# Kernel optimization log

Hardware: AMD Instinct MI355X
Metric: run time of the kernel (lower is better)

## Reference

```python
import jax, jax.numpy as jnp
import numpy as np

B, T, C, H = 2, 2048, 1024, 16
HD = C // H  # head_dim = 64

def _rope(x, cos, sin):
    # x: [B,H,T,HD]; cos/sin: [T,HD//2]
    x2 = x.reshape(*x.shape[:-1], HD // 2, 2)
    x0, x1 = x2[..., 0], x2[..., 1]
    # complex multiply (x0 + i x1) * (cos + i sin)
    o0 = x0 * cos - x1 * sin
    o1 = x0 * sin + x1 * cos
    return jnp.stack([o0, o1], axis=-1).reshape(x.shape)

def setup_inputs() -> dict:
    key = jax.random.key(0)
    k1, k2, k3 = jax.random.split(key, 3)
    x = jax.random.normal(k1, (B, T, C), dtype=jnp.float32)
    w_qkv = jax.random.normal(k2, (C, 3 * C), dtype=jnp.float32) * (1.0 / np.sqrt(C))
    w_proj = jax.random.normal(k3, (C, C), dtype=jnp.float32) * (1.0 / np.sqrt(C))
    # standard RoPE frequencies: theta_j = 10000^(-2j/HD), angles t*theta_j
    inv_freq = 1.0 / (10000.0 ** (np.arange(0, HD, 2, dtype=np.float32) / HD))  # [HD//2]
    ang = np.arange(T, dtype=np.float32)[:, None] * inv_freq[None, :]           # [T,HD//2]
    return {"x": x, "w_qkv": w_qkv, "w_proj": w_proj,
            "freqs_cos": jnp.asarray(np.cos(ang)), "freqs_sin": jnp.asarray(np.sin(ang))}

def reference(x, w_qkv, w_proj, freqs_cos, freqs_sin):
    qkv = x @ w_qkv                                   # [B,T,3C]
    q, k, v = jnp.split(qkv, 3, axis=-1)
    def heads(t):
        return t.reshape(B, T, H, HD).transpose(0, 2, 1, 3)  # [B,H,T,HD]
    q, k, v = heads(q), heads(k), heads(v)
    q = _rope(q, freqs_cos, freqs_sin)
    k = _rope(k, freqs_cos, freqs_sin)
    scores = jnp.einsum('bhqd,bhkd->bhqk', q, k) * (1.0 / np.sqrt(HD))
    causal = jnp.tril(jnp.ones((T, T), dtype=bool))
    scores = jnp.where(causal, scores, jnp.finfo(scores.dtype).min)
    attn = jax.nn.softmax(scores, axis=-1)
    y = jnp.einsum('bhqk,bhkd->bhqd', attn, v)        # [B,H,T,HD]
    y = y.transpose(0, 2, 1, 3).reshape(B, T, C)
    return y @ w_proj
```

## Files before the change

kernel.cpp:

```cpp
#include <hip/hip_runtime.h>

typedef float  floatx4 __attribute__((ext_vector_type(4)));
typedef _Float16 half8 __attribute__((ext_vector_type(8)));
typedef _Float16 half4v __attribute__((ext_vector_type(4)));
typedef _Float16 half2v __attribute__((ext_vector_type(2)));

__device__ __forceinline__ void gld16(const void* g, void* l) {
    __builtin_amdgcn_global_load_lds(
        (const __attribute__((address_space(1))) void*)g,
        (__attribute__((address_space(3))) void*)l, 16, 0, 0);
}

__global__ __launch_bounds__(256) void conv_x_kernel(const float* __restrict__ x,
                                                     _Float16* __restrict__ xh) {
    int i = blockIdx.x * 256 + threadIdx.x;
    float4 v = ((const float4*)x)[i];
    half4v o = { (_Float16)v.x, (_Float16)v.y, (_Float16)v.z, (_Float16)v.w };
    ((half4v*)xh)[i] = o;
}

__global__ __launch_bounds__(256) void transpose_f32f16(const float* __restrict__ W,
                                                        _Float16* __restrict__ WT,
                                                        int K, int N) {
    __shared__ _Float16 t[64][72];
    int n0 = blockIdx.x * 64, k0 = blockIdx.y * 64;
    int c = threadIdx.x & 63, r4 = threadIdx.x >> 6;
    for (int rr = 0; rr < 64; rr += 4) {
        int k = k0 + rr + r4;
        t[rr + r4][c] = (_Float16)W[(size_t)k * N + n0 + c];
    }
    __syncthreads();
    for (int rr = 0; rr < 64; rr += 4) {
        int n = n0 + rr + r4;
        WT[(size_t)n * K + k0 + c] = t[c][rr + r4];
    }
}

__global__ __launch_bounds__(256) void gemm_tn(const _Float16* __restrict__ A,
                                               const _Float16* __restrict__ BT,
                                               _Float16* __restrict__ Cf16,
                                               float* __restrict__ Cf32,
                                               int M, int N, int K) {
    __shared__ __align__(16) _Float16 sAB[2 * 128 * 32];
    _Float16* sA = sAB;
    _Float16* sB = sAB + 128 * 32;

    const int tid  = threadIdx.x;
    const int wave = tid >> 6, lane = tid & 63;
    const int lrow = lane & 15, quad = lane >> 4;
    const int bm = blockIdx.x * 128, bn = blockIdx.y * 128;
    const int waveM = (wave >> 1) * 64, waveN = (wave & 1) * 64;

    floatx4 acc[4][4] = {};

    const int r0 = tid >> 2,          k80 = (tid & 3) * 8;
    const int r1 = (tid + 256) >> 2,  k81 = ((tid + 256) & 3) * 8;
    _Float16* lA0 = sA + (wave * 64) * 8;
    _Float16* lA1 = sA + (wave * 64 + 256) * 8;
    _Float16* lB0 = sB + (wave * 64) * 8;
    _Float16* lB1 = sB + (wave * 64 + 256) * 8;
    const _Float16* A0 = A + (size_t)(bm + r0) * K + k80;
    const _Float16* A1 = A + (size_t)(bm + r1) * K + k81;
    const _Float16* B0 = BT + (size_t)(bn + r0) * K + k80;
    const _Float16* B1 = BT + (size_t)(bn + r1) * K + k81;

    for (int k0 = 0; k0 < K; k0 += 32) {
        gld16(A0 + k0, lA0);
        gld16(A1 + k0, lA1);
        gld16(B0 + k0, lB0);
        gld16(B1 + k0, lB1);
        __syncthreads();

        half8 aF[4], bF[4];
#pragma unroll
        for (int mt = 0; mt < 4; ++mt)
            aF[mt] = *(const half8*)&sA[(waveM + mt * 16 + lrow) * 32 + quad * 8];
#pragma unroll
        for (int nt = 0; nt < 4; ++nt)
            bF[nt] = *(const half8*)&sB[(waveN + nt * 16 + lrow) * 32 + quad * 8];
#pragma unroll
        for (int mt = 0; mt < 4; ++mt)
#pragma unroll
            for (int nt = 0; nt < 4; ++nt)
                acc[mt][nt] = __builtin_amdgcn_mfma_f32_16x16x32_f16(
                    aF[mt], bF[nt], acc[mt][nt], 0, 0, 0);
        __syncthreads();
    }

    if (Cf16) {
        const int PS = 132;
#pragma unroll
        for (int pass = 0; pass < 4; ++pass) {
            if ((wave >> 1) == (pass >> 1)) {
#pragma unroll
                for (int mt2 = 0; mt2 < 2; ++mt2) {
                    int mt = (pass & 1) * 2 + mt2;
#pragma unroll
                    for (int nt = 0; nt < 4; ++nt)
#pragma unroll
                        for (int r = 0; r < 4; ++r)
                            sAB[(mt2 * 16 + quad * 4 + r) * PS + waveN + nt * 16 + lrow] =
                                (_Float16)acc[mt][nt][r];
                }
            }
            __syncthreads();
            {
                int row = tid >> 3, c0 = (tid & 7) * 16;
                const uint4* src = (const uint4*)&sAB[row * PS + c0];
                uint4 d0 = src[0], d1 = src[1];
                uint4* dst = (uint4*)&Cf16[(size_t)(bm + pass * 32 + row) * N + bn + c0];
                dst[0] = d0; dst[1] = d1;
            }
            __syncthreads();
        }
    } else {
#pragma unroll
        for (int mt = 0; mt < 4; ++mt)
#pragma unroll
            for (int nt = 0; nt < 4; ++nt)
#pragma unroll
                for (int r = 0; r < 4; ++r) {
                    int row = bm + waveM + mt * 16 + quad * 4 + r;
                    int col = bn + waveN + nt * 16 + lrow;
                    Cf32[(size_t)row * N + col] = acc[mt][nt][r];
                }
    }
}

__global__ __launch_bounds__(256) void rope_vt(const _Float16* __restrict__ qkv,
                                               const float* __restrict__ fc,
                                               const float* __restrict__ fs,
                                               _Float16* __restrict__ qh,
                                               _Float16* __restrict__ kh,
                                               _Float16* __restrict__ vt) {
    __shared__ _Float16 s[64][72];
    const int bh = blockIdx.y, b = bh >> 4, h = bh & 15;
    const int t0 = blockIdx.x * 64;
    const int tid = threadIdx.x;

    {
        int c4 = (tid & 15) * 4;
        int j0 = c4 >> 1;
        int rr = tid >> 4;
#pragma unroll
        for (int pass = 0; pass < 4; ++pass) {
            int tt = t0 + pass * 16 + rr;
            const _Float16* src = qkv + (size_t)(b * 2048 + tt) * 3072 + h * 64 + c4;
            float c0 = fc[tt * 32 + j0],     s0 = fs[tt * 32 + j0];
            float c1 = fc[tt * 32 + j0 + 1], s1 = fs[tt * 32 + j0 + 1];
            half4v qv = *(const half4v*)(src);
            half4v kv = *(const half4v*)(src + 1024);
            half4v qo, ko;
            {
                float x0 = (float)qv[0], x1 = (float)qv[1];
                qo[0] = (_Float16)(x0 * c0 - x1 * s0); qo[1] = (_Float16)(x0 * s0 + x1 * c0);
                x0 = (float)qv[2]; x1 = (float)qv[3];
                qo[2] = (_Float16)(x0 * c1 - x1 * s1); qo[3] = (_Float16)(x0 * s1 + x1 * c1);
                x0 = (float)kv[0]; x1 = (float)kv[1];
                ko[0] = (_Float16)(x0 * c0 - x1 * s0); ko[1] = (_Float16)(x0 * s0 + x1 * c0);
                x0 = (float)kv[2]; x1 = (float)kv[3];
                ko[2] = (_Float16)(x0 * c1 - x1 * s1); ko[3] = (_Float16)(x0 * s1 + x1 * c1);
            }
            size_t o = ((size_t)bh * 2048 + tt) * 64 + c4;
            *(half4v*)&qh[o] = qo;
            *(half4v*)&kh[o] = ko;
        }
    }
    {
        int c = tid & 63, r4 = tid >> 6;
        const _Float16* srcv = qkv + 2048 + h * 64;
        for (int rr = 0; rr < 64; rr += 4)
            s[rr + r4][c] = srcv[(size_t)(b * 2048 + t0 + rr + r4) * 3072 + c];
        __syncthreads();
        for (int rr = 0; rr < 64; rr += 4)
            vt[((size_t)bh * 64 + rr + r4) * 2048 + t0 + c] = s[c][rr + r4];
    }
}

__global__ __launch_bounds__(256, 6) void attn_sk(const _Float16* __restrict__ Q,
                                                  const _Float16* __restrict__ Kk,
                                                  const _Float16* __restrict__ Vt,
                                                  _Float16* __restrict__ Y,
                                                  _Float16* __restrict__ Opart,
                                                  float* __restrict__ lpart) {
    __shared__ __align__(16) _Float16 sK[64 * 64];
    __shared__ __align__(16) _Float16 sV[64 * 64];
    __shared__ __align__(16) _Float16 sP[64 * 72];

    const int bh = blockIdx.x, b = bh >> 4, h = bh & 15;
    const int u = blockIdx.y;
    int qt, k0, k1, slot = 0; bool direct;
    if (u < 16)              { qt = 16 + u;  k0 = 0;  k1 = 15; direct = false; slot = (qt - 16) * 2; }
    else { int i = (u - 16) >> 1;
        if (((u - 16) & 1) == 0) { qt = 15 - i; k0 = 0;  k1 = qt; direct = true; }
        else                     { qt = 31 - i; k0 = 16; k1 = qt; direct = false; slot = (qt - 16) * 2 + 1; }
    }

    const int tid = threadIdx.x;
    const int wave = tid >> 6, lane = tid & 63;
    const int lq = lane & 15, quad = lane >> 4;

    const _Float16* Kbase = Kk + (size_t)bh * 2048 * 64;
    const _Float16* Vbase = Vt + (size_t)bh * 64 * 2048;

    const _Float16 qscale = (_Float16)(0.125f * 1.44269504f);
    half8 qF[2];
    {
        const _Float16* Qp = Q + ((size_t)bh * 2048 + qt * 64 + wave * 16 + lq) * 64;
#pragma unroll
        for (int ks = 0; ks < 2; ++ks)
            qF[ks] = (*(const half8*)(Qp + ks * 32 + quad * 8)) * qscale;
    }

    floatx4 O[4] = {};
    float lacc = 0.f;

    for (int kt = k0; kt <= k1; ++kt) {
        const _Float16* kb = Kbase + (size_t)kt * 64 * 64;
        const _Float16* vb = Vbase + kt * 64;
#pragma unroll
        for (int hlf = 0; hlf < 2; ++hlf) {
            int s = tid + hlf * 256;
            int row = s >> 3;
            int ccg = (s & 7) ^ (row & 7);
            gld16(kb + row * 64 + ccg * 8, sK + s * 8);
            gld16(vb + (size_t)row * 2048 + ccg * 8, sV + s * 8);
        }
        __syncthreads();

        floatx4 St[4];
#pragma unroll
        for (int kt4 = 0; kt4 < 4; ++kt4) {
            floatx4 s = { -12.f, -12.f, -12.f, -12.f };
#pragma unroll
            for (int ks = 0; ks < 2; ++ks) {
                half8 kf = *(const half8*)&sK[(kt4 * 16 + lq) * 64 +
                                              (((ks * 4 + quad) ^ (lq & 7)) * 8)];
                s = __builtin_amdgcn_mfma_f32_16x16x32_f16(kf, qF[ks], s, 0, 0, 0);
            }
            St[kt4] = s;
        }
        if (kt == qt) {
#pragma unroll
            for (int kt4 = 0; kt4 < 4; ++kt4)
#pragma unroll
                for (int r = 0; r < 4; ++r)
                    if (kt4 * 16 + quad * 4 + r > wave * 16 + lq) St[kt4][r] = -1e30f;
        }
#pragma unroll
        for (int kt4 = 0; kt4 < 4; ++kt4)
#pragma unroll
            for (int r = 0; r < 4; ++r)
                St[kt4][r] = __builtin_amdgcn_exp2f(St[kt4][r]);
        lacc += (St[0][0] + St[0][1] + St[0][2] + St[0][3])
              + (St[1][0] + St[1][1] + St[1][2] + St[1][3])
              + (St[2][0] + St[2][1] + St[2][2] + St[2][3])
              + (St[3][0] + St[3][1] + St[3][2] + St[3][3]);

        _Float16* pw = (_Float16*)&sP[(wave * 16 + lq) * 72];
#pragma unroll
        for (int kt4 = 0; kt4 < 4; ++kt4) {
            half4v pk = { (_Float16)St[kt4][0], (_Float16)St[kt4][1],
                          (_Float16)St[kt4][2], (_Float16)St[kt4][3] };
            *(half4v*)(pw + kt4 * 16 + quad * 4) = pk;
        }
        half8 aP[2];
#pragma unroll
        for (int ks = 0; ks < 2; ++ks)
            aP[ks] = *(const half8*)(pw + ks * 32 + quad * 8);
#pragma unroll
        for (int nt = 0; nt < 4; ++nt)
#pragma unroll
            for (int ks = 0; ks < 2; ++ks) {
                half8 vf = *(const half8*)&sV[(nt * 16 + lq) * 64 +
                                              (((ks * 4 + quad) ^ (lq & 7)) * 8)];
                O[nt] = __builtin_amdgcn_mfma_f32_16x16x32_f16(aP[ks], vf, O[nt], 0, 0, 0);
            }
        __syncthreads();
    }

    float l = lacc;
    l += __shfl_xor(l, 16);
    l += __shfl_xor(l, 32);

    if (direct) {
        float invl = 1.0f / l;
#pragma unroll
        for (int r = 0; r < 4; ++r) {
            float iv = __shfl(invl, (lane & 48) | (quad * 4 + r));
            int q = qt * 64 + wave * 16 + quad * 4 + r;
            size_t rowoff = ((size_t)b * 2048 + q) * 1024 + h * 64;
#pragma unroll
            for (int nt = 0; nt < 4; ++nt)
                Y[rowoff + nt * 16 + lq] = (_Float16)(O[nt][r] * iv);
        }
    } else {
        int gslot = bh * 32 + slot;
        _Float16* op = Opart + (size_t)gslot * 4096;
#pragma unroll
        for (int r = 0; r < 4; ++r) {
            int row = wave * 16 + quad * 4 + r;
#pragma unroll
            for (int nt = 0; nt < 4; ++nt)
                op[row * 64 + nt * 16 + lq] = (_Float16)O[nt][r];
        }
        if (quad == 0)
            lpart[gslot * 64 + wave * 16 + lq] = l;
    }
}

__global__ __launch_bounds__(256) void attn_reduce(const _Float16* __restrict__ Opart,
                                                   const float* __restrict__ lpart,
                                                   _Float16* __restrict__ Y) {
    const int bh = blockIdx.x, b = bh >> 4, h = bh & 15;
    const int qx = blockIdx.y, qt = 16 + qx;
    const int g0 = (bh * 16 + qx) * 2, g1 = g0 + 1;
    const int t = threadIdx.x;
    const int row = t >> 2, cs = (t & 3) * 16;

    const _Float16* p0 = Opart + (size_t)g0 * 4096 + row * 64 + cs;
    const _Float16* p1 = Opart + (size_t)g1 * 4096 + row * 64 + cs;
    float invl = 1.0f / (lpart[g0 * 64 + row] + lpart[g1 * 64 + row]);

    half8 a0 = *(const half8*)p0, a1 = *(const half8*)(p0 + 8);
    half8 b0 = *(const half8*)p1, b1 = *(const half8*)(p1 + 8);
    half8 o0, o1;
#pragma unroll
    for (int i = 0; i < 8; ++i) {
        o0[i] = (_Float16)(((float)a0[i] + (float)b0[i]) * invl);
        o1[i] = (_Float16)(((float)a1[i] + (float)b1[i]) * invl);
    }
    _Float16* y = Y + ((size_t)b * 2048 + qt * 64 + row) * 1024 + h * 64 + cs;
    *(half8*)y = o0;
    *(half8*)(y + 8) = o1;
}

extern "C" void kernel_launch(void* const* d_in, const int* in_sizes, int n_in,
                              void* d_out, int out_size, void* d_ws, size_t ws_size,
                              hipStream_t stream) {
    const float* x     = (const float*)d_in[0];
    const float* wqkv  = (const float*)d_in[1];
    const float* wproj = (const float*)d_in[2];
    const float* fc    = (const float*)d_in[3];
    const float* fs    = (const float*)d_in[4];
    float* out = (float*)d_out;

    char* ws = (char*)d_ws;
    _Float16* xh    = (_Float16*)(ws);
    _Float16* wqT   = (_Float16*)(ws + ((size_t)8  << 20));
    _Float16* wpT   = (_Float16*)(ws + ((size_t)14 << 20));
    _Float16* qkvh  = (_Float16*)(ws + ((size_t)16 << 20));
    _Float16* qh    = (_Float16*)(ws + ((size_t)40 << 20));
    _Float16* kh    = (_Float16*)(ws + ((size_t)48 << 20));
    _Float16* vt    = (_Float16*)(ws + ((size_t)56 << 20));
    _Float16* yh    = xh;
    _Float16* Opart = qkvh;
    float*    lpartf= (float*)(ws + ((size_t)26 << 20));

    conv_x_kernel<<<4096, 256, 0, stream>>>(x, xh);
    transpose_f32f16<<<dim3(48, 16), 256, 0, stream>>>(wqkv, wqT, 1024, 3072);
    transpose_f32f16<<<dim3(16, 16), 256, 0, stream>>>(wproj, wpT, 1024, 1024);
    gemm_tn<<<dim3(32, 24), 256, 0, stream>>>(xh, wqT, qkvh, nullptr, 4096, 3072, 1024);
    rope_vt<<<dim3(32, 32), 256, 0, stream>>>(qkvh, fc, fs, qh, kh, vt);
    attn_sk<<<dim3(32, 48), 256, 0, stream>>>(qh, kh, vt, yh, Opart, lpartf);
    attn_reduce<<<dim3(32, 16), 256, 0, stream>>>(Opart, lpartf, yh);
    gemm_tn<<<dim3(32, 8), 256, 0, stream>>>(yh, wpT, nullptr, out, 4096, 1024, 1024);
}
```

Baseline: 196.7 us.

## Process two query tiles per attention block, add 64-row output GEMM, per-wave epilogue

The attention kernel now handles a 128-row query chunk (two 64-row tiles) per block, sharing each loaded K/V tile between both, with a table-driven split-K schedule and a matching reduce kernel. The output projection uses a new 64x128-tile GEMM so more blocks fill the device. The QKV GEMM epilogue is replaced with a per-wave LDS staging path that avoids block-wide barriers. These changes reduce K/V reloads and barrier overhead, at the cost of higher register pressure (launch bounds lowered to 3) and fewer attention blocks.

```diff
diff --git a/kernel.cpp b/kernel.cpp
--- a/kernel.cpp
+++ b/kernel.cpp
@@ -3,7 +3,6 @@
 typedef float  floatx4 __attribute__((ext_vector_type(4)));
 typedef _Float16 half8 __attribute__((ext_vector_type(8)));
 typedef _Float16 half4v __attribute__((ext_vector_type(4)));
-typedef _Float16 half2v __attribute__((ext_vector_type(2)));
 
 __device__ __forceinline__ void gld16(const void* g, void* l) {
     __builtin_amdgcn_global_load_lds(
@@ -39,7 +38,6 @@
 __global__ __launch_bounds__(256) void gemm_tn(const _Float16* __restrict__ A,
                                                const _Float16* __restrict__ BT,
                                                _Float16* __restrict__ Cf16,
-                                               float* __restrict__ Cf32,
                                                int M, int N, int K) {
     __shared__ __align__(16) _Float16 sAB[2 * 128 * 32];
     _Float16* sA = sAB;
@@ -87,44 +85,82 @@
         __syncthreads();
     }
 
-    if (Cf16) {
-        const int PS = 132;
-#pragma unroll
-        for (int pass = 0; pass < 4; ++pass) {
-            if ((wave >> 1) == (pass >> 1)) {
-#pragma unroll
-                for (int mt2 = 0; mt2 < 2; ++mt2) {
-                    int mt = (pass & 1) * 2 + mt2;
-#pragma unroll
-                    for (int nt = 0; nt < 4; ++nt)
-#pragma unroll
-                        for (int r = 0; r < 4; ++r)
-                            sAB[(mt2 * 16 + quad * 4 + r) * PS + waveN + nt * 16 + lrow] =
-                                (_Float16)acc[mt][nt][r];
-                }
-            }
-            __syncthreads();
-            {
-                int row = tid >> 3, c0 = (tid & 7) * 16;
-                const uint4* src = (const uint4*)&sAB[row * PS + c0];
-                uint4 d0 = src[0], d1 = src[1];
-                uint4* dst = (uint4*)&Cf16[(size_t)(bm + pass * 32 + row) * N + bn + c0];
-                dst[0] = d0; dst[1] = d1;
-            }
-            __syncthreads();
-        }
-    } else {
-#pragma unroll
-        for (int mt = 0; mt < 4; ++mt)
+    _Float16* ep = sAB + wave * 1152;
+    const int erow = lane >> 3, ecol = (lane & 7) * 8;
+#pragma unroll
+    for (int mt = 0; mt < 4; ++mt) {
+#pragma unroll
+        for (int nt = 0; nt < 4; ++nt)
+#pragma unroll
+            for (int r = 0; r < 4; ++r)
+                ep[(quad * 4 + r) * 72 + nt * 16 + lrow] = (_Float16)acc[mt][nt][r];
+        __builtin_amdgcn_wave_barrier();
+#pragma unroll
+        for (int st = 0; st < 2; ++st) {
+            uint4 d = *(const uint4*)&ep[(st * 8 + erow) * 72 + ecol];
+            *(uint4*)&Cf16[(size_t)(bm + waveM + mt * 16 + st * 8 + erow) * N +
+                           bn + waveN + ecol] = d;
+        }
+        __builtin_amdgcn_wave_barrier();
+    }
+}
+
+__global__ __launch_bounds__(256) void gemm_tn64(const _Float16* __restrict__ A,
+                                                 const _Float16* __restrict__ BT,
+                                                 float* __restrict__ C,
+                                                 int M, int N, int K) {
+    __shared__ __align__(16) _Float16 sA[64 * 32];
+    __shared__ __align__(16) _Float16 sB[128 * 32];
+
+    const int tid  = threadIdx.x;
+    const int wave = tid >> 6, lane = tid & 63;
+    const int lrow = lane & 15, quad = lane >> 4;
+    const int bm = blockIdx.x * 64, bn = blockIdx.y * 128;
+    const int waveM = (wave >> 1) * 32, waveN = (wave & 1) * 64;
+
+    floatx4 acc[2][4] = {};
+
+    const int ra = tid >> 2, k8 = (tid & 3) * 8;
+    const int rb1 = (tid + 256) >> 2, k8b = ((tid + 256) & 3) * 8;
+    const _Float16* Ap  = A + (size_t)(bm + ra) * K + k8;
+    const _Float16* Bp0 = BT + (size_t)(bn + ra) * K + k8;
+    const _Float16* Bp1 = BT + (size_t)(bn + rb1) * K + k8b;
+    _Float16* lA  = sA + tid * 8;
+    _Float16* lB0 = sB + (wave * 64) * 8;
+    _Float16* lB1 = sB + (wave * 64 + 256) * 8;
+
+    for (int k0 = 0; k0 < K; k0 += 32) {
+        gld16(Ap + k0, lA);
+        gld16(Bp0 + k0, lB0);
+        gld16(Bp1 + k0, lB1);
+        __syncthreads();
+
+        half8 aF[2], bF[4];
+#pragma unroll
+        for (int mt = 0; mt < 2; ++mt)
+            aF[mt] = *(const half8*)&sA[(waveM + mt * 16 + lrow) * 32 + quad * 8];
+#pragma unroll
+        for (int nt = 0; nt < 4; ++nt)
+            bF[nt] = *(const half8*)&sB[(waveN + nt * 16 + lrow) * 32 + quad * 8];
+#pragma unroll
+        for (int mt = 0; mt < 2; ++mt)
 #pragma unroll
             for (int nt = 0; nt < 4; ++nt)
-#pragma unroll
-                for (int r = 0; r < 4; ++r) {
-                    int row = bm + waveM + mt * 16 + quad * 4 + r;
-                    int col = bn + waveN + nt * 16 + lrow;
-                    Cf32[(size_t)row * N + col] = acc[mt][nt][r];
-                }
-    }
+                acc[mt][nt] = __builtin_amdgcn_mfma_f32_16x16x32_f16(
+                    aF[mt], bF[nt], acc[mt][nt], 0, 0, 0);
+        __syncthreads();
+    }
+
+#pragma unroll
+    for (int mt = 0; mt < 2; ++mt)
+#pragma unroll
+        for (int nt = 0; nt < 4; ++nt)
+#pragma unroll
+            for (int r = 0; r < 4; ++r) {
+                int row = bm + waveM + mt * 16 + quad * 4 + r;
+                int col = bn + waveN + nt * 16 + lrow;
+                C[(size_t)row * N + col] = acc[mt][nt][r];
+            }
 }
 
 __global__ __launch_bounds__(256) void rope_vt(const _Float16* __restrict__ qkv,
@@ -177,24 +213,34 @@
     }
 }
 
-__global__ __launch_bounds__(256, 6) void attn_sk(const _Float16* __restrict__ Q,
-                                                  const _Float16* __restrict__ Kk,
-                                                  const _Float16* __restrict__ Vt,
-                                                  _Float16* __restrict__ Y,
-                                                  _Float16* __restrict__ Opart,
-                                                  float* __restrict__ lpart) {
+#define U_(qc,k0,k1,dir,slot) ((qc)|((k0)<<5)|((k1)<<11)|((dir)<<17)|((slot)<<18))
+__device__ const unsigned int UTAB[24] = {
+    U_(15, 0,15,0,14), U_(15,16,31,0,15), U_( 7, 0,15,1, 0),
+    U_(14, 0,14,0,12), U_(14,15,29,0,13),
+    U_(13, 0,13,0,10), U_(13,14,27,0,11), U_( 6, 0,13,1, 0),
+    U_(12, 0,12,0, 8), U_(12,13,25,0, 9),
+    U_(11, 0,11,0, 6), U_(11,12,23,0, 7), U_( 5, 0,11,1, 0),
+    U_(10, 0,10,0, 4), U_(10,11,21,0, 5),
+    U_( 9, 0, 9,0, 2), U_( 9,10,19,0, 3), U_( 4, 0, 9,1, 0),
+    U_( 8, 0, 8,0, 0), U_( 8, 9,17,0, 1),
+    U_( 3, 0, 7,1, 0), U_( 2, 0, 5,1, 0), U_( 1, 0, 3,1, 0), U_( 0, 0, 1,1, 0)
+};
+
+__global__ __launch_bounds__(256, 3) void attn_sk2(const _Float16* __restrict__ Q,
+                                                   const _Float16* __restrict__ Kk,
+                                                   const _Float16* __restrict__ Vt,
+                                                   _Float16* __restrict__ Y,
+                                                   _Float16* __restrict__ Opart,
+                                                   float* __restrict__ lpart) {
     __shared__ __align__(16) _Float16 sK[64 * 64];
     __shared__ __align__(16) _Float16 sV[64 * 64];
-    __shared__ __align__(16) _Float16 sP[64 * 72];
+    __shared__ __align__(16) _Float16 sP[128 * 72];
 
     const int bh = blockIdx.x, b = bh >> 4, h = bh & 15;
-    const int u = blockIdx.y;
-    int qt, k0, k1, slot = 0; bool direct;
-    if (u < 16)              { qt = 16 + u;  k0 = 0;  k1 = 15; direct = false; slot = (qt - 16) * 2; }
-    else { int i = (u - 16) >> 1;
-        if (((u - 16) & 1) == 0) { qt = 15 - i; k0 = 0;  k1 = qt; direct = true; }
-        else                     { qt = 31 - i; k0 = 16; k1 = qt; direct = false; slot = (qt - 16) * 2 + 1; }
-    }
+    const unsigned e = UTAB[blockIdx.y];
+    const int qc = e & 31, k0 = (e >> 5) & 63, k1 = (e >> 11) & 63;
+    const int dir = (e >> 17) & 1, slot = (e >> 18) & 15;
+    const int d0 = 2 * qc, d1 = 2 * qc + 1;
 
     const int tid = threadIdx.x;
     const int wave = tid >> 6, lane = tid & 63;
@@ -204,18 +250,20 @@
     const _Float16* Vbase = Vt + (size_t)bh * 64 * 2048;
 
     const _Float16 qscale = (_Float16)(0.125f * 1.44269504f);
-    half8 qF[2];
-    {
-        const _Float16* Qp = Q + ((size_t)bh * 2048 + qt * 64 + wave * 16 + lq) * 64;
+    half8 qF[2][2];
+#pragma unroll
+    for (int g = 0; g < 2; ++g) {
+        const _Float16* Qp = Q + ((size_t)bh * 2048 + qc * 128 + g * 64 + wave * 16 + lq) * 64;
 #pragma unroll
         for (int ks = 0; ks < 2; ++ks)
-            qF[ks] = (*(const half8*)(Qp + ks * 32 + quad * 8)) * qscale;
-    }
-
-    floatx4 O[4] = {};
-    float lacc = 0.f;
+            qF[g][ks] = (*(const half8*)(Qp + ks * 32 + quad * 8)) * qscale;
+    }
+
+    floatx4 O0[4] = {}, O1[4] = {};
+    float lacc0 = 0.f, lacc1 = 0.f;
 
     for (int kt = k0; kt <= k1; ++kt) {
+        const bool live0 = (kt <= d0);
         const _Float16* kb = Kbase + (size_t)kt * 64 * 64;
         const _Float16* vb = Vbase + kt * 64;
 #pragma unroll
@@ -228,111 +276,132 @@
         }
         __syncthreads();
 
-        floatx4 St[4];
+        half4v P0[4], P1[4];
 #pragma unroll
         for (int kt4 = 0; kt4 < 4; ++kt4) {
-            floatx4 s = { -12.f, -12.f, -12.f, -12.f };
-#pragma unroll
-            for (int ks = 0; ks < 2; ++ks) {
-                half8 kf = *(const half8*)&sK[(kt4 * 16 + lq) * 64 +
-                                              (((ks * 4 + quad) ^ (lq & 7)) * 8)];
-                s = __builtin_amdgcn_mfma_f32_16x16x32_f16(kf, qF[ks], s, 0, 0, 0);
-            }
-            St[kt4] = s;
-        }
-        if (kt == qt) {
+            half8 kf0 = *(const half8*)&sK[(kt4 * 16 + lq) * 64 + ((quad ^ (lq & 7)) * 8)];
+            half8 kf1 = *(const half8*)&sK[(kt4 * 16 + lq) * 64 + (((4 + quad) ^ (lq & 7)) * 8)];
+            floatx4 s1 = { -12.f, -12.f, -12.f, -12.f };
+            s1 = __builtin_amdgcn_mfma_f32_16x16x32_f16(kf0, qF[1][0], s1, 0, 0, 0);
+            s1 = __builtin_amdgcn_mfma_f32_16x16x32_f16(kf1, qF[1][1], s1, 0, 0, 0);
+            if (kt == d1) {
+#pragma unroll
+                for (int r = 0; r < 4; ++r)
+                    if (kt4 * 16 + quad * 4 + r > wave * 16 + lq) s1[r] = -1e30f;
+            }
+#pragma unroll
+            for (int r = 0; r < 4; ++r) s1[r] = __builtin_amdgcn_exp2f(s1[r]);
+            lacc1 += s1[0] + s1[1] + s1[2] + s1[3];
+            P1[kt4] = half4v{ (_Float16)s1[0], (_Float16)s1[1],
+                              (_Float16)s1[2], (_Float16)s1[3] };
+            if (live0) {
+                floatx4 s0 = { -12.f, -12.f, -12.f, -12.f };
+                s0 = __builtin_amdgcn_mfma_f32_16x16x32_f16(kf0, qF[0][0], s0, 0, 0, 0);
+                s0 = __builtin_amdgcn_mfma_f32_16x16x32_f16(kf1, qF[0][1], s0, 0, 0, 0);
+                if (kt == d0) {
+#pragma unroll
+                    for (int r = 0; r < 4; ++r)
+                        if (kt4 * 16 + quad * 4 + r > wave * 16 + lq) s0[r] = -1e30f;
+                }
+#pragma unroll
+                for (int r = 0; r < 4; ++r) s0[r] = __builtin_amdgcn_exp2f(s0[r]);
+                lacc0 += s0[0] + s0[1] + s0[2] + s0[3];
+                P0[kt4] = half4v{ (_Float16)s0[0], (_Float16)s0[1],
+                                  (_Float16)s0[2], (_Float16)s0[3] };
+            }
+        }
+
+        _Float16* pw1 = &sP[(64 + wave * 16 + lq) * 72];
+#pragma unroll
+        for (int kt4 = 0; kt4 < 4; ++kt4)
+            *(half4v*)(pw1 + kt4 * 16 + quad * 4) = P1[kt4];
+        _Float16* pw0 = &sP[(wave * 16 + lq) * 72];
+        if (live0) {
 #pragma unroll
             for (int kt4 = 0; kt4 < 4; ++kt4)
-#pragma unroll
-                for (int r = 0; r < 4; ++r)
-                    if (kt4 * 16 + quad * 4 + r > wave * 16 + lq) St[kt4][r] = -1e30f;
-        }
-#pragma unroll
-        for (int kt4 = 0; kt4 < 4; ++kt4)
-#pragma unroll
-            for (int r = 0; r < 4; ++r)
-                St[kt4][r] = __builtin_amdgcn_exp2f(St[kt4][r]);
-        lacc += (St[0][0] + St[0][1] + St[0][2] + St[0][3])
-              + (St[1][0] + St[1][1] + St[1][2] + St[1][3])
-              + (St[2][0] + St[2][1] + St[2][2] + St[2][3])
-              + (St[3][0] + St[3][1] + St[3][2] + St[3][3]);
-
-        _Float16* pw = (_Float16*)&sP[(wave * 16 + lq) * 72];
-#pragma unroll
-        for (int kt4 = 0; kt4 < 4; ++kt4) {
-            half4v pk = { (_Float16)St[kt4][0], (_Float16)St[kt4][1],
-                          (_Float16)St[kt4][2], (_Float16)St[kt4][3] };
-            *(half4v*)(pw + kt4 * 16 + quad * 4) = pk;
-        }
-        half8 aP[2];
-#pragma unroll
-        for (int ks = 0; ks < 2; ++ks)
-            aP[ks] = *(const half8*)(pw + ks * 32 + quad * 8);
+                *(half4v*)(pw0 + kt4 * 16 + quad * 4) = P0[kt4];
+        }
+        __builtin_amdgcn_wave_barrier();
+
+        half8 aP0[2], aP1[2];
+#pragma unroll
+        for (int ks = 0; ks < 2; ++ks) {
+            aP1[ks] = *(const half8*)(pw1 + ks * 32 + quad * 8);
+            if (live0) aP0[ks] = *(const half8*)(pw0 + ks * 32 + quad * 8);
+        }
 #pragma unroll
         for (int nt = 0; nt < 4; ++nt)
 #pragma unroll
             for (int ks = 0; ks < 2; ++ks) {
                 half8 vf = *(const half8*)&sV[(nt * 16 + lq) * 64 +
                                               (((ks * 4 + quad) ^ (lq & 7)) * 8)];
-                O[nt] = __builtin_amdgcn_mfma_f32_16x16x32_f16(aP[ks], vf, O[nt], 0, 0, 0);
-            }
-        __syncthreads();
-    }
-
-    float l = lacc;
-    l += __shfl_xor(l, 16);
-    l += __shfl_xor(l, 32);
-
-    if (direct) {
-        float invl = 1.0f / l;
-#pragma unroll
-        for (int r = 0; r < 4; ++r) {
-            float iv = __shfl(invl, (lane & 48) | (quad * 4 + r));
-            int q = qt * 64 + wave * 16 + quad * 4 + r;
-            size_t rowoff = ((size_t)b * 2048 + q) * 1024 + h * 64;
-#pragma unroll
-            for (int nt = 0; nt < 4; ++nt)
-                Y[rowoff + nt * 16 + lq] = (_Float16)(O[nt][r] * iv);
-        }
-    } else {
-        int gslot = bh * 32 + slot;
-        _Float16* op = Opart + (size_t)gslot * 4096;
-#pragma unroll
-        for (int r = 0; r < 4; ++r) {
-            int row = wave * 16 + quad * 4 + r;
-#pragma unroll
-            for (int nt = 0; nt < 4; ++nt)
-                op[row * 64 + nt * 16 + lq] = (_Float16)O[nt][r];
-        }
-        if (quad == 0)
-            lpart[gslot * 64 + wave * 16 + lq] = l;
-    }
-}
-
-__global__ __launch_bounds__(256) void attn_reduce(const _Float16* __restrict__ Opart,
-                                                   const float* __restrict__ lpart,
-                                                   _Float16* __restrict__ Y) {
+                O1[nt] = __builtin_amdgcn_mfma_f32_16x16x32_f16(aP1[ks], vf, O1[nt], 0, 0, 0);
+                if (live0)
+                    O0[nt] = __builtin_amdgcn_mfma_f32_16x16x32_f16(aP0[ks], vf, O0[nt], 0, 0, 0);
+            }
+        __syncthreads();
+    }
+
+#pragma unroll
+    for (int g = 0; g < 2; ++g) {
+        float l = g ? lacc1 : lacc0;
+        l += __shfl_xor(l, 16);
+        l += __shfl_xor(l, 32);
+        floatx4* O = g ? O1 : O0;
+        if (dir) {
+            float invl = 1.0f / l;
+#pragma unroll
+            for (int r = 0; r < 4; ++r) {
+                float iv = __shfl(invl, (lane & 48) | (quad * 4 + r));
+                int q = qc * 128 + g * 64 + wave * 16 + quad * 4 + r;
+                size_t rowoff = ((size_t)b * 2048 + q) * 1024 + h * 64;
+#pragma unroll
+                for (int nt = 0; nt < 4; ++nt)
+                    Y[rowoff + nt * 16 + lq] = (_Float16)(O[nt][r] * iv);
+            }
+        } else {
+            int gslot = bh * 16 + slot;
+            _Float16* op = Opart + (size_t)gslot * 8192;
+#pragma unroll
+            for (int r = 0; r < 4; ++r) {
+                int row = g * 64 + wave * 16 + quad * 4 + r;
+#pragma unroll
+                for (int nt = 0; nt < 4; ++nt)
+                    op[row * 64 + nt * 16 + lq] = (_Float16)O[nt][r];
+            }
+            if (quad == 0)
+                lpart[gslot * 128 + g * 64 + wave * 16 + lq] = l;
+        }
+    }
+}
+
+__global__ __launch_bounds__(256) void attn_reduce2(const _Float16* __restrict__ Opart,
+                                                    const float* __restrict__ lpart,
+                                                    _Float16* __restrict__ Y) {
     const int bh = blockIdx.x, b = bh >> 4, h = bh & 15;
-    const int qx = blockIdx.y, qt = 16 + qx;
-    const int g0 = (bh * 16 + qx) * 2, g1 = g0 + 1;
-    const int t = threadIdx.x;
-    const int row = t >> 2, cs = (t & 3) * 16;
-
-    const _Float16* p0 = Opart + (size_t)g0 * 4096 + row * 64 + cs;
-    const _Float16* p1 = Opart + (size_t)g1 * 4096 + row * 64 + cs;
-    float invl = 1.0f / (lpart[g0 * 64 + row] + lpart[g1 * 64 + row]);
-
-    half8 a0 = *(const half8*)p0, a1 = *(const half8*)(p0 + 8);
-    half8 b0 = *(const half8*)p1, b1 = *(const half8*)(p1 + 8);
-    half8 o0, o1;
-#pragma unroll
-    for (int i = 0; i < 8; ++i) {
-        o0[i] = (_Float16)(((float)a0[i] + (float)b0[i]) * invl);
-        o1[i] = (_Float16)(((float)a1[i] + (float)b1[i]) * invl);
-    }
-    _Float16* y = Y + ((size_t)b * 2048 + qt * 64 + row) * 1024 + h * 64 + cs;
-    *(half8*)y = o0;
-    *(half8*)(y + 8) = o1;
+    const int qcx = blockIdx.y, qc = 8 + qcx;
+    const int g0 = bh * 16 + qcx * 2, g1 = g0 + 1;
+    const int tid = threadIdx.x;
+
+#pragma unroll
+    for (int it = 0; it < 2; ++it) {
+        int idx = tid + it * 256;
+        int row = idx >> 2, cs = (idx & 3) * 16;
+        const _Float16* p0 = Opart + (size_t)g0 * 8192 + row * 64 + cs;
+        const _Float16* p1 = Opart + (size_t)g1 * 8192 + row * 64 + cs;
+        float invl = 1.0f / (lpart[g0 * 128 + row] + lpart[g1 * 128 + row]);
+        half8 a0 = *(const half8*)p0, a1 = *(const half8*)(p0 + 8);
+        half8 b0 = *(const half8*)p1, b1 = *(const half8*)(p1 + 8);
+        half8 o0, o1;
+#pragma unroll
+        for (int i = 0; i < 8; ++i) {
+            o0[i] = (_Float16)(((float)a0[i] + (float)b0[i]) * invl);
+            o1[i] = (_Float16)(((float)a1[i] + (float)b1[i]) * invl);
+        }
+        _Float16* y = Y + ((size_t)b * 2048 + qc * 128 + row) * 1024 + h * 64 + cs;
+        *(half8*)y = o0;
+        *(half8*)(y + 8) = o1;
+    }
 }
 
 extern "C" void kernel_launch(void* const* d_in, const int* in_sizes, int n_in,
@@ -360,9 +429,9 @@
     conv_x_kernel<<<4096, 256, 0, stream>>>(x, xh);
     transpose_f32f16<<<dim3(48, 16), 256, 0, stream>>>(wqkv, wqT, 1024, 3072);
     transpose_f32f16<<<dim3(16, 16), 256, 0, stream>>>(wproj, wpT, 1024, 1024);
-    gemm_tn<<<dim3(32, 24), 256, 0, stream>>>(xh, wqT, qkvh, nullptr, 4096, 3072, 1024);
+    gemm_tn<<<dim3(32, 24), 256, 0, stream>>>(xh, wqT, qkvh, 4096, 3072, 1024);
     rope_vt<<<dim3(32, 32), 256, 0, stream>>>(qkvh, fc, fs, qh, kh, vt);
-    attn_sk<<<dim3(32, 48), 256, 0, stream>>>(qh, kh, vt, yh, Opart, lpartf);
-    attn_reduce<<<dim3(32, 16), 256, 0, stream>>>(Opart, lpartf, yh);
-    gemm_tn<<<dim3(32, 8), 256, 0, stream>>>(yh, wpT, nullptr, out, 4096, 1024, 1024);
-}
+    attn_sk2<<<dim3(32, 24), 256, 0, stream>>>(qh, kh, vt, yh, Opart, lpartf);
+    attn_reduce2<<<dim3(32, 8), 256, 0, stream>>>(Opart, lpartf, yh);
+    gemm_tn64<<<dim3(64, 8), 256, 0, stream>>>(yh, wpT, out, 4096, 1024, 1024);
+}
```

Result: faster. 190.5 us (-3.1%).
